# Performance work log

Measured on AMD Instinct MI355X. Metric: run time of the kernel, lower is better.

The kernel has to match this reference:

```python
import jax, jax.numpy as jnp
import numpy as np

N = 2048      # agent_num
H = 2048      # hid_size
OBS = 1024    # obs_size
A = 64        # action_dim
ITERS = 3     # comm_iters
B = 1         # batch (structurally 1: original does gate.view(1,n,n))
STD = 0.02


def setup_inputs() -> dict:
    key = jax.random.key(0)
    ks = jax.random.split(key, 10)
    f = lambda k, shp: (jax.random.normal(k, shp, jnp.float32) * STD)
    return {
        "obs": jax.random.normal(ks[0], (B, N, OBS), jnp.float32),
        "alive_mask": jnp.ones((N,), jnp.float32),
        "enc_w": f(ks[1], (H, OBS)),
        "enc_b": jnp.zeros((H,), jnp.float32),
        "g_w": f(ks[2], (N, H)),
        "g_b": jnp.zeros((N,), jnp.float32),
        "w_ih": f(ks[3], (4 * H, H)),
        "w_hh": f(ks[4], (4 * H, H)),
        "b_ih": f(ks[5], (4 * H,)),
        "b_hh": f(ks[6], (4 * H,)),
        "act_w": f(ks[7], (A, H)),
        "act_b": jnp.zeros((A,), jnp.float32),
        "val_w": f(ks[8], (1, H)),
        "val_b": jnp.zeros((1,), jnp.float32),
    }


def reference(obs, alive_mask, enc_w, enc_b, g_w, g_b, w_ih, w_hh,
              b_ih, b_hh, act_w, act_b, val_w, val_b):
    b, n, _ = obs.shape
    hid = enc_w.shape[0]
    # state encoder: tanh(Linear(obs))
    e = jnp.tanh(jnp.einsum('bno,ho->bnh', obs, enc_w) + enc_b)  # (B,n,H)
    h = jnp.zeros((b, n, hid), obs.dtype)
    cell = jnp.zeros((b, n, hid), obs.dtype)
    comm_mask = 1.0 - jnp.eye(n, dtype=obs.dtype)                # (n,n), no self-comm
    n_alive = jnp.sum(alive_mask)
    alive_pair = alive_mask[:, None] * alive_mask[None, :]       # alive[j]*alive[i]
    static_w = comm_mask * alive_pair / (n_alive - 1.0)          # (n,n)

    for it in range(ITERS):
        # hard gate: ceil(sigmoid(g(h)))  -> (B, n_sender, n_receiver)
        gate = jnp.ceil(jax.nn.sigmoid(jnp.einsum('bjh,kh->bjk', h, g_w) + g_b))
        G = gate * static_w                                      # (B,n,n)
        # masked gated broadcast-sum over sender agents j (fused, no (B,n,n,H))
        if it == 0:
            c = jnp.zeros_like(h)
        else:
            c = jnp.einsum('bji,bjh->bih', G, h)
        inp = e + c                                              # (B,n,H)
        # torch.nn.LSTMCell, gate order (i, f, g, o)
        z = (jnp.einsum('bnh,gh->bng', inp, w_ih)
             + jnp.einsum('bnh,gh->bng', h, w_hh) + b_ih + b_hh)
        zi, zf, zg, zo = jnp.split(z, 4, axis=-1)
        cell = jax.nn.sigmoid(zf) * cell + jax.nn.sigmoid(zi) * jnp.tanh(zg)
        h = jax.nn.sigmoid(zo) * jnp.tanh(cell)

    log_p = jax.nn.log_softmax(jnp.einsum('bnh,ah->bna', h, act_w) + act_b, axis=-1)
    value = jnp.einsum('bnh,vh->bnv', h, val_w) + val_b
    return log_p, value
```

## Files before the change

### kernel.cpp

```cpp
#include <hip/hip_runtime.h>
#include <cmath>

#define N_AG 2048
#define HID  2048
#define OBSD 1024
#define ACT  64
#define GATES (4*HID)

typedef short s16x8 __attribute__((ext_vector_type(8)));
typedef short s16x4 __attribute__((ext_vector_type(4)));
typedef float f32x4 __attribute__((ext_vector_type(4)));

__device__ __forceinline__ unsigned short f2bf(float f) {
  union { float f; unsigned u; } v; v.f = f;
  return (unsigned short)((v.u + 0x7FFFu + ((v.u >> 16) & 1u)) >> 16);
}
__device__ __forceinline__ float bf2f(unsigned short u) {
  union { float f; unsigned u; } v; v.u = ((unsigned)u) << 16;
  return v.f;
}
__device__ __forceinline__ float sigm(float x) { return 1.0f / (1.0f + expf(-x)); }

__device__ __forceinline__ void gload16(const unsigned short* g, unsigned short* l) {
  __builtin_amdgcn_global_load_lds(
      (const __attribute__((address_space(1))) void*)g,
      (__attribute__((address_space(3))) void*)l, 16, 0, 0);
}

__global__ __launch_bounds__(512, 2) void gemm256(
    const unsigned short* __restrict__ A, const unsigned short* __restrict__ B,
    int K, int lda, int ldb, unsigned short* __restrict__ C, int ldc)
{
  __shared__ __align__(16) unsigned short As[32768];
  __shared__ __align__(16) unsigned short Bs[32768];

  const int tid  = threadIdx.x;
  const int lane = tid & 63;
  const int wave = tid >> 6;
  const int wm   = wave >> 2, wn = wave & 3;
  const int quad = lane >> 4, l16 = lane & 15, r7 = lane & 7;
  const long tileM = (long)blockIdx.y * 256;
  const long tileN = (long)blockIdx.x * 256;

  const unsigned scol  = (((lane & 7) ^ (lane >> 3)) * 8u);
  const unsigned aoffL = (unsigned)(tileM + wave * 8 + (lane >> 3)) * (unsigned)lda + scol;
  const unsigned boffL = (unsigned)(tileN + (wave >> 2) * 64 + (wave & 3) * 8 + (lane >> 3))
                           * (unsigned)ldb + scol;

#define ST_A(d, h, t) { \
    gload16(A + aoffL + (unsigned)((h) * 64) * (unsigned)lda + (unsigned)(t) * 64u, \
            &As[(d) * 16384 + (h) * 8192 + wave * 512]); \
    gload16(A + aoffL + (unsigned)(128 + (h) * 64) * (unsigned)lda + (unsigned)(t) * 64u, \
            &As[(d) * 16384 + (h) * 8192 + wave * 512 + 4096]); }
#define ST_B(d, h, t) { \
    gload16(B + boffL + (unsigned)((h) * 32) * (unsigned)ldb + (unsigned)(t) * 64u, \
            &Bs[(d) * 16384 + (h) * 8192 + wave * 512]); \
    gload16(B + boffL + (unsigned)(128 + (h) * 32) * (unsigned)ldb + (unsigned)(t) * 64u, \
            &Bs[(d) * 16384 + (h) * 8192 + wave * 512 + 4096]); }

  const int ax = wm * 4096 + l16 * 64;
  const int bx = wn * 2048 + l16 * 64;
  const int c0 = (quad ^ r7) * 8;
  const int c1 = ((4 + quad) ^ r7) * 8;

  s16x8 af0[4][2], af1[4][2], bA[2][2], bB[2][2];
  f32x4 acc[8][4] = {};

#define LD_A(d, Mh, dst) { const unsigned short* p_ = &As[(d) * 16384 + (Mh) * 8192 + ax]; \
    _Pragma("unroll") for (int ml = 0; ml < 4; ++ml) { \
      dst[ml][0] = *(const s16x8*)(p_ + ml * 1024 + c0); \
      dst[ml][1] = *(const s16x8*)(p_ + ml * 1024 + c1); } }
#define LD_B(d, Nh, dst) { const unsigned short* p_ = &Bs[(d) * 16384 + (Nh) * 8192 + bx]; \
    _Pragma("unroll") for (int nl = 0; nl < 2; ++nl) { \
      dst[nl][0] = *(const s16x8*)(p_ + nl * 1024 + c0); \
      dst[nl][1] = *(const s16x8*)(p_ + nl * 1024 + c1); } }
#define QMM(Mh, Nh, afv, bb) \
    _Pragma("unroll") for (int ks = 0; ks < 2; ++ks) \
    _Pragma("unroll") for (int ml = 0; ml < 4; ++ml) \
    _Pragma("unroll") for (int nl = 0; nl < 2; ++nl) \
      acc[(Mh) * 4 + ml][(Nh) * 2 + nl] = __builtin_amdgcn_mfma_f32_16x16x32_bf16( \
          afv[ml][ks], bb[nl][ks], acc[(Mh) * 4 + ml][(Nh) * 2 + nl], 0, 0, 0);
#define BAR  __builtin_amdgcn_s_barrier()
#define SCHB __builtin_amdgcn_sched_barrier(0)

  const int NT = K >> 6;

  ST_B(0, 0, 0); ST_A(0, 0, 0); ST_B(0, 1, 0); ST_A(0, 1, 0);
  asm volatile("s_waitcnt vmcnt(0)" ::: "memory");
  BAR;
  LD_A(0, 0, af0); LD_B(0, 0, bA);

  for (int t = 0; t < NT; ++t) {
    const int cur = t & 1, nxt = cur ^ 1;
    const bool s1 = (t + 1 < NT);
    LD_B(cur, 1, bB);
    if (s1) { ST_B(nxt, 0, t + 1); ST_A(nxt, 0, t + 1); }
    SCHB;
    __builtin_amdgcn_s_setprio(1); QMM(0, 0, af0, bA); __builtin_amdgcn_s_setprio(0);
    if (s1) { asm volatile("s_waitcnt vmcnt(4)" ::: "memory"); }
    else    { asm volatile("s_waitcnt vmcnt(0)" ::: "memory"); }
    BAR;
    LD_A(cur, 1, af1);
    if (s1) ST_B(nxt, 1, t + 1);
    SCHB;
    __builtin_amdgcn_s_setprio(1); QMM(0, 1, af0, bB); __builtin_amdgcn_s_setprio(0);
    if (s1) { asm volatile("s_waitcnt vmcnt(2)" ::: "memory"); }
    BAR;
    if (s1) ST_A(nxt, 1, t + 1);
    SCHB;
    __builtin_amdgcn_s_setprio(1); QMM(1, 0, af1, bA); __builtin_amdgcn_s_setprio(0);
    if (s1) LD_B(nxt, 0, bA);
    BAR;
    if (s1) LD_A(nxt, 0, af0);
    SCHB;
    __builtin_amdgcn_s_setprio(1); QMM(1, 1, af1, bB); __builtin_amdgcn_s_setprio(0);
    if (s1) { asm volatile("s_waitcnt vmcnt(2)" ::: "memory"); }
    BAR;
  }

#pragma unroll
  for (int mf = 0; mf < 8; ++mf) {
    long r0 = tileM + wm * 128 + mf * 16 + quad * 4;
#pragma unroll
    for (int nf = 0; nf < 4; ++nf) {
      long col = tileN + wn * 64 + nf * 16 + l16;
#pragma unroll
      for (int r = 0; r < 4; ++r)
        C[(r0 + r) * ldc + col] = f2bf(acc[mf][nf][r]);
    }
  }
#undef ST_A
#undef ST_B
#undef LD_A
#undef LD_B
#undef QMM
#undef BAR
#undef SCHB
}

template <int MODE>
__global__ __launch_bounds__(256, 4) void gemm_bt(
    const unsigned short* __restrict__ A, const unsigned short* __restrict__ B,
    int K, int lda, int ldb,
    unsigned short* __restrict__ Cb, float* __restrict__ Cf, int ldc,
    const float* __restrict__ bias)
{
  __shared__ __align__(16) unsigned short As0[2 * 128 * 32];
  __shared__ __align__(16) unsigned short Bs0[2 * 128 * 32];
  const int tid  = threadIdx.x;
  const int lane = tid & 63;
  const int wave = tid >> 6;
  const int wm = wave >> 1, wn = wave & 1;
  const int quad = lane >> 4, l16 = lane & 15;
  const long tileM = (long)blockIdx.y * 128;
  const long tileN = (long)blockIdx.x * 128;

  const int srow = lane >> 2;
  const int skc  = (lane & 3) * 8;
  const unsigned short* gA = &A[(tileM + wave * 32 + srow) * lda + skc];
  const unsigned short* gB = &B[(tileN + wave * 32 + srow) * ldb + skc];
  const int ldsOff = wave * 32 * 32;

  f32x4 acc[4][4] = {};
  const int nIt = K >> 5;

  gload16(gA, &As0[ldsOff]);
  gload16(gA + 16 * lda, &As0[ldsOff + 16 * 32]);
  gload16(gB, &Bs0[ldsOff]);
  gload16(gB + 16 * ldb, &Bs0[ldsOff + 16 * 32]);

  for (int i = 0; i < nIt; ++i) {
    __syncthreads();
    const int cb = (i & 1) * 4096;
    if (i + 1 < nIt) {
      const int nb = ((i + 1) & 1) * 4096;
      const long ko = (long)(i + 1) * 32;
      gload16(gA + ko, &As0[nb + ldsOff]);
      gload16(gA + ko + 16 * lda, &As0[nb + ldsOff + 16 * 32]);
      gload16(gB + ko, &Bs0[nb + ldsOff]);
      gload16(gB + ko + 16 * ldb, &Bs0[nb + ldsOff + 16 * 32]);
    }
    s16x8 af[4], bfr[4];
#pragma unroll
    for (int ii = 0; ii < 4; ++ii)
      af[ii] = *(const s16x8*)&As0[cb + (wm * 64 + ii * 16 + l16) * 32 + quad * 8];
#pragma unroll
    for (int j = 0; j < 4; ++j)
      bfr[j] = *(const s16x8*)&Bs0[cb + (wn * 64 + j * 16 + l16) * 32 + quad * 8];
#pragma unroll
    for (int ii = 0; ii < 4; ++ii)
#pragma unroll
      for (int j = 0; j < 4; ++j)
        acc[ii][j] = __builtin_amdgcn_mfma_f32_16x16x32_bf16(af[ii], bfr[j], acc[ii][j], 0, 0, 0);
  }

#pragma unroll
  for (int i = 0; i < 4; ++i) {
    long r0 = tileM + wm * 64 + i * 16 + quad * 4;
#pragma unroll
    for (int j = 0; j < 4; ++j) {
      long col = tileN + wn * 64 + j * 16 + l16;
      float bv = (MODE == 1) ? bias[col] : 0.f;
#pragma unroll
      for (int r = 0; r < 4; ++r) {
        float v = acc[i][j][r];
        if (MODE == 1) v = tanhf(v + bv);
        if (MODE == 2) Cf[(r0 + r) * ldc + col] = v;
        else           Cb[(r0 + r) * ldc + col] = f2bf(v);
      }
    }
  }
}

__global__ void cvt4_dual(const float* __restrict__ inA, unsigned short* __restrict__ outA,
                          const float* __restrict__ inB, unsigned short* __restrict__ outB) {
  int i = blockIdx.x * 256 + threadIdx.x;
  f32x4 a = ((const f32x4*)inA)[i];
  f32x4 b = ((const f32x4*)inB)[i];
  s16x4 oa, ob;
#pragma unroll
  for (int c = 0; c < 4; ++c) { oa[c] = (short)f2bf(a[c]); ob[c] = (short)f2bf(b[c]); }
  ((s16x4*)outA)[i] = oa;
  ((s16x4*)outB)[i] = ob;
}

__global__ void buildw(const float* __restrict__ w_ih, const float* __restrict__ w_hh,
                       const float* __restrict__ nA,
                       unsigned short* __restrict__ Wihb, unsigned short* __restrict__ W2b) {
  int i = blockIdx.x * 256 + threadIdx.x;
  float s = 1.0f / (nA[0] - 1.0f);
  size_t off = (size_t)i * 4;
  f32x4 a = *(const f32x4*)&w_ih[off];
  f32x4 b = *(const f32x4*)&w_hh[off];
  s16x4 oa, ob;
#pragma unroll
  for (int c = 0; c < 4; ++c) {
    oa[c] = (short)f2bf(a[c]);
    ob[c] = (short)f2bf(b[c] - s * a[c]);
  }
  *(s16x4*)&Wihb[off] = oa;
  *(s16x4*)&W2b[off] = ob;
}

__global__ void build_whd(const float* __restrict__ act_w, const float* __restrict__ val_w,
                          unsigned short* __restrict__ whd) {
  int i = blockIdx.x * 256 + threadIdx.x;
  int r = i >> 9;
  int k = (i & 511) * 4;
  f32x4 v = {0.f, 0.f, 0.f, 0.f};
  if (r < 64)       v = *(const f32x4*)&act_w[(size_t)r * HID + k];
  else if (r == 64) v = *(const f32x4*)&val_w[k];
  s16x4 o;
  o[0] = (short)f2bf(v[0]); o[1] = (short)f2bf(v[1]);
  o[2] = (short)f2bf(v[2]); o[3] = (short)f2bf(v[3]);
  *(s16x4*)&whd[(size_t)r * HID + k] = o;
}

__global__ void biasmix(const float* __restrict__ b_ih, const float* __restrict__ b_hh,
                        float* __restrict__ bc) {
  int i = blockIdx.x * 256 + threadIdx.x;
  if (i < GATES) bc[i] = b_ih[i] + b_hh[i];
}

__global__ void nalive_k(const float* __restrict__ alive, float* __restrict__ nA) {
  __shared__ float red[256];
  float s = 0.f;
  for (int i = threadIdx.x; i < N_AG; i += 256) s += alive[i];
  red[threadIdx.x] = s;
  __syncthreads();
  for (int st = 128; st > 0; st >>= 1) {
    if (threadIdx.x < st) red[threadIdx.x] += red[threadIdx.x + st];
    __syncthreads();
  }
  if (threadIdx.x == 0) nA[0] = red[0];
}

__global__ void colsum(const unsigned short* __restrict__ hb, const float* __restrict__ alive,
                       float* __restrict__ S) {
  int hid = blockIdx.x * 256 + threadIdx.x;
  int r0 = blockIdx.y * 128;
  float s = 0.f;
  for (int n = r0; n < r0 + 128; ++n) s += alive[n] * bf2f(hb[(size_t)n * HID + hid]);
  atomicAdd(&S[hid], s);
}

__global__ __launch_bounds__(256) void gemv_q(const unsigned short* __restrict__ Wihb,
                                              const float* __restrict__ S,
                                              const float* __restrict__ nA,
                                              float* __restrict__ q) {
  __shared__ float Sl[HID];
  int tid = threadIdx.x, lane = tid & 63, wave = tid >> 6;
  for (int k = tid; k < HID; k += 256) Sl[k] = S[k];
  __syncthreads();
  int g = blockIdx.x * 4 + wave;
  const unsigned short* wr = Wihb + (size_t)g * HID;
  float acc = 0.f;
#pragma unroll
  for (int c = 0; c < 4; ++c) {
    int k = c * 512 + lane * 8;
    s16x8 w = *(const s16x8*)&wr[k];
#pragma unroll
    for (int e = 0; e < 8; ++e) acc += bf2f((unsigned short)w[e]) * Sl[k + e];
  }
  for (int off = 32; off; off >>= 1) acc += __shfl_xor(acc, off);
  if (lane == 0) q[g] = acc / (nA[0] - 1.0f);
}

__global__ void lstm_k(const unsigned short* __restrict__ zb, const unsigned short* __restrict__ E1b,
                       const float* __restrict__ q, const float* __restrict__ bc,
                       float* __restrict__ cell, unsigned short* __restrict__ hb, int first) {
  int i = blockIdx.x * 256 + threadIdx.x;
  int n = i >> 9;
  int hid = (i & 511) * 4;
  size_t base = (size_t)n * GATES;
  float zt[4][4];
#pragma unroll
  for (int t = 0; t < 4; ++t) {
    int off = t * HID + hid;
    s16x4 e1 = *(const s16x4*)&E1b[base + off];
    f32x4 bcv = *(const f32x4*)&bc[off];
#pragma unroll
    for (int c = 0; c < 4; ++c) zt[t][c] = bf2f((unsigned short)e1[c]) + bcv[c];
    if (!first) {
      s16x4 z2 = *(const s16x4*)&zb[base + off];
      f32x4 qv = *(const f32x4*)&q[off];
#pragma unroll
      for (int c = 0; c < 4; ++c) zt[t][c] += bf2f((unsigned short)z2[c]) + qv[c];
    }
  }
  f32x4 cold = {0.f, 0.f, 0.f, 0.f};
  if (!first) cold = ((const f32x4*)cell)[i];
  f32x4 cnew; s16x4 xb;
#pragma unroll
  for (int c = 0; c < 4; ++c) {
    float ig = sigm(zt[0][c]);
    float fg = sigm(zt[1][c]);
    float gg = tanhf(zt[2][c]);
    float og = sigm(zt[3][c]);
    cnew[c] = fg * cold[c] + ig * gg;
    float hv = og * tanhf(cnew[c]);
    xb[c] = (short)f2bf(hv);
  }
  ((f32x4*)cell)[i] = cnew;
  *(s16x4*)&hb[(size_t)n * HID + hid] = xb;
}

__global__ __launch_bounds__(256) void head_ep(const float* __restrict__ zh,
                                               const float* __restrict__ act_b,
                                               const float* __restrict__ val_b,
                                               float* __restrict__ out) {
  int wave = threadIdx.x >> 6, lane = threadIdx.x & 63;
  int row = blockIdx.x * 4 + wave;
  const float* zr = zh + (size_t)row * 128;
  float a = zr[lane] + act_b[lane];
  float m = a;
  for (int off = 32; off; off >>= 1) m = fmaxf(m, __shfl_xor(m, off));
  float ex = expf(a - m), s = ex;
  for (int off = 32; off; off >>= 1) s += __shfl_xor(s, off);
  out[(size_t)row * ACT + lane] = a - m - logf(s);
  if (lane == 0) out[(size_t)N_AG * ACT + row] = zr[64] + val_b[0];
}

extern "C" void kernel_launch(void* const* d_in, const int* in_sizes, int n_in,
                              void* d_out, int out_size, void* d_ws, size_t ws_size,
                              hipStream_t stream) {
  const float* obs   = (const float*)d_in[0];
  const float* alive = (const float*)d_in[1];
  const float* enc_w = (const float*)d_in[2];
  const float* enc_b = (const float*)d_in[3];
  const float* w_ih  = (const float*)d_in[6];
  const float* w_hh  = (const float*)d_in[7];
  const float* b_ih  = (const float*)d_in[8];
  const float* b_hh  = (const float*)d_in[9];
  const float* act_w = (const float*)d_in[10];
  const float* act_b = (const float*)d_in[11];
  const float* val_w = (const float*)d_in[12];
  const float* val_b = (const float*)d_in[13];
  float* out = (float*)d_out;

  char* p = (char*)d_ws;
  unsigned short* Wihb = (unsigned short*)p; p += (size_t)GATES * HID * 2;
  unsigned short* W2b  = (unsigned short*)p; p += (size_t)GATES * HID * 2;
  unsigned short* E1b  = (unsigned short*)p; p += (size_t)N_AG * GATES * 2;
  unsigned short* zb   = (unsigned short*)p; p += (size_t)N_AG * GATES * 2;
  unsigned short* obsb = (unsigned short*)p; p += (size_t)N_AG * OBSD * 2;
  unsigned short* encb = (unsigned short*)p; p += (size_t)HID * OBSD * 2;
  unsigned short* eb   = (unsigned short*)p; p += (size_t)N_AG * HID * 2;
  unsigned short* hb   = (unsigned short*)p; p += (size_t)N_AG * HID * 2;
  unsigned short* Whd  = (unsigned short*)p; p += (size_t)128 * HID * 2;
  float* cell = (float*)p; p += (size_t)N_AG * HID * 4;
  float* zh   = (float*)p; p += (size_t)N_AG * 128 * 4;
  float* bc   = (float*)p; p += GATES * 4;
  float* q    = (float*)p; p += GATES * 4;
  float* S    = (float*)p; p += HID * 4;
  float* nA   = (float*)p; p += 256;

  cvt4_dual<<<(N_AG * OBSD / 4) / 256, 256, 0, stream>>>(obs, obsb, enc_w, encb);
  nalive_k<<<1, 256, 0, stream>>>(alive, nA);
  buildw<<<((size_t)GATES * HID / 4) / 256, 256, 0, stream>>>(w_ih, w_hh, nA, Wihb, W2b);
  build_whd<<<(128 * HID / 4) / 256, 256, 0, stream>>>(act_w, val_w, Whd);
  biasmix<<<GATES / 256, 256, 0, stream>>>(b_ih, b_hh, bc);

  gemm_bt<1><<<dim3(HID / 128, N_AG / 128), 256, 0, stream>>>(
      obsb, encb, OBSD, OBSD, OBSD, eb, nullptr, HID, enc_b);

  gemm256<<<dim3(GATES / 256, N_AG / 256), 512, 0, stream>>>(
      eb, Wihb, HID, HID, HID, E1b, GATES);
  lstm_k<<<(N_AG * HID / 4) / 256, 256, 0, stream>>>(nullptr, E1b, nullptr, bc, cell, hb, 1);

  for (int it = 1; it < 3; ++it) {
    hipMemsetAsync(S, 0, HID * 4, stream);
    colsum<<<dim3(HID / 256, 16), 256, 0, stream>>>(hb, alive, S);
    gemv_q<<<GATES / 4, 256, 0, stream>>>(Wihb, S, nA, q);
    gemm256<<<dim3(GATES / 256, N_AG / 256), 512, 0, stream>>>(
        hb, W2b, HID, HID, HID, zb, GATES);
    lstm_k<<<(N_AG * HID / 4) / 256, 256, 0, stream>>>(zb, E1b, q, bc, cell, hb, 0);
  }

  gemm_bt<2><<<dim3(1, N_AG / 128), 256, 0, stream>>>(
      hb, Whd, HID, HID, HID, nullptr, zh, 128, nullptr);
  head_ep<<<N_AG / 4, 256, 0, stream>>>(zh, act_b, val_b, out);
}
```

Before: 565.1 us.

## Fuse LSTM cell update into gate GEMM epilogue via interleaved weight layout

Reorders the rows of the input and recurrent weights and the combined bias so that each 64-column slice of a GEMM tile holds the i, f, g, o gates for the same 16 hidden units. The LSTM cell update then runs in the GEMM epilogue, which removes the separate lstm kernel and the bf16 round trip through the z buffer. h is double-buffered because the GEMM now writes new h while other blocks still read the old h. The head GEMM is also split along K into 8 chunks that accumulate with atomics, so it launches more blocks; the price is an extra memset and float atomics.

```diff
diff --git a/kernel.cpp b/kernel.cpp
--- a/kernel.cpp
+++ b/kernel.cpp
@@ -27,9 +27,14 @@
       (__attribute__((address_space(3))) void*)l, 16, 0, 0);
 }
 
+
+template <int MODE>
 __global__ __launch_bounds__(512, 2) void gemm256(
     const unsigned short* __restrict__ A, const unsigned short* __restrict__ B,
-    int K, int lda, int ldb, unsigned short* __restrict__ C, int ldc)
+    int K, int lda, int ldb,
+    unsigned short* __restrict__ E1b, const float* __restrict__ q,
+    const float* __restrict__ bc, float* __restrict__ cell,
+    unsigned short* __restrict__ hN)
 {
   __shared__ __align__(16) unsigned short As[32768];
   __shared__ __align__(16) unsigned short Bs[32768];
@@ -118,15 +123,40 @@
     BAR;
   }
 
+  const int cb0 = (int)tileN + wn * 64;
+  const int hid = ((cb0 >> 6) << 4) | l16;
+  float bcv[4], qv[4];
+#pragma unroll
+  for (int g = 0; g < 4; ++g) {
+    bcv[g] = bc[cb0 + g * 16 + l16];
+    qv[g]  = (MODE == 11) ? q[cb0 + g * 16 + l16] : 0.f;
+  }
 #pragma unroll
   for (int mf = 0; mf < 8; ++mf) {
-    long r0 = tileM + wm * 128 + mf * 16 + quad * 4;
-#pragma unroll
-    for (int nf = 0; nf < 4; ++nf) {
-      long col = tileN + wn * 64 + nf * 16 + l16;
-#pragma unroll
-      for (int r = 0; r < 4; ++r)
-        C[(r0 + r) * ldc + col] = f2bf(acc[mf][nf][r]);
+    long ag0 = tileM + wm * 128 + mf * 16 + quad * 4;
+#pragma unroll
+    for (int r = 0; r < 4; ++r) {
+      long ag = ag0 + r;
+      size_t eb_i = (size_t)ag * GATES + cb0 + l16;
+      float zi = acc[mf][0][r], zf = acc[mf][1][r];
+      float zg = acc[mf][2][r], zo = acc[mf][3][r];
+      if (MODE == 10) {
+        E1b[eb_i]      = f2bf(zi);
+        E1b[eb_i + 16] = f2bf(zf);
+        E1b[eb_i + 32] = f2bf(zg);
+        E1b[eb_i + 48] = f2bf(zo);
+        zi += bcv[0]; zf += bcv[1]; zg += bcv[2]; zo += bcv[3];
+      } else {
+        zi += bf2f(E1b[eb_i])      + qv[0] + bcv[0];
+        zf += bf2f(E1b[eb_i + 16]) + qv[1] + bcv[1];
+        zg += bf2f(E1b[eb_i + 32]) + qv[2] + bcv[2];
+        zo += bf2f(E1b[eb_i + 48]) + qv[3] + bcv[3];
+      }
+      float cold = (MODE == 10) ? 0.f : cell[(size_t)ag * HID + hid];
+      float cnew = sigm(zf) * cold + sigm(zi) * tanhf(zg);
+      float hv   = sigm(zo) * tanhf(cnew);
+      cell[(size_t)ag * HID + hid] = cnew;
+      hN[(size_t)ag * HID + hid]   = f2bf(hv);
     }
   }
 #undef ST_A
@@ -154,11 +184,12 @@
   const int quad = lane >> 4, l16 = lane & 15;
   const long tileM = (long)blockIdx.y * 128;
   const long tileN = (long)blockIdx.x * 128;
+  const long koff  = (long)blockIdx.z * K;
 
   const int srow = lane >> 2;
   const int skc  = (lane & 3) * 8;
-  const unsigned short* gA = &A[(tileM + wave * 32 + srow) * lda + skc];
-  const unsigned short* gB = &B[(tileN + wave * 32 + srow) * ldb + skc];
+  const unsigned short* gA = &A[(tileM + wave * 32 + srow) * lda + koff + skc];
+  const unsigned short* gB = &B[(tileN + wave * 32 + srow) * ldb + koff + skc];
   const int ldsOff = wave * 32 * 32;
 
   f32x4 acc[4][4] = {};
@@ -204,9 +235,8 @@
 #pragma unroll
       for (int r = 0; r < 4; ++r) {
         float v = acc[i][j][r];
-        if (MODE == 1) v = tanhf(v + bv);
-        if (MODE == 2) Cf[(r0 + r) * ldc + col] = v;
-        else           Cb[(r0 + r) * ldc + col] = f2bf(v);
+        if (MODE == 1) { v = tanhf(v + bv); Cb[(r0 + r) * ldc + col] = f2bf(v); }
+        if (MODE == 2) atomicAdd(&Cf[(r0 + r) * ldc + col], v);
       }
     }
   }
@@ -229,17 +259,22 @@
                        unsigned short* __restrict__ Wihb, unsigned short* __restrict__ W2b) {
   int i = blockIdx.x * 256 + threadIdx.x;
   float s = 1.0f / (nA[0] - 1.0f);
-  size_t off = (size_t)i * 4;
-  f32x4 a = *(const f32x4*)&w_ih[off];
-  f32x4 b = *(const f32x4*)&w_hh[off];
+  int c  = i >> 9;
+  int kk = (i & 511) * 4;
+  int g   = (c >> 4) & 3;
+  int hid = ((c >> 6) << 4) | (c & 15);
+  size_t src = ((size_t)g * HID + hid) * HID + kk;
+  size_t dst = (size_t)c * HID + kk;
+  f32x4 a = *(const f32x4*)&w_ih[src];
+  f32x4 b = *(const f32x4*)&w_hh[src];
   s16x4 oa, ob;
 #pragma unroll
-  for (int c = 0; c < 4; ++c) {
-    oa[c] = (short)f2bf(a[c]);
-    ob[c] = (short)f2bf(b[c] - s * a[c]);
-  }
-  *(s16x4*)&Wihb[off] = oa;
-  *(s16x4*)&W2b[off] = ob;
+  for (int e = 0; e < 4; ++e) {
+    oa[e] = (short)f2bf(a[e]);
+    ob[e] = (short)f2bf(b[e] - s * a[e]);
+  }
+  *(s16x4*)&Wihb[dst] = oa;
+  *(s16x4*)&W2b[dst] = ob;
 }
 
 __global__ void build_whd(const float* __restrict__ act_w, const float* __restrict__ val_w,
@@ -259,7 +294,12 @@
 __global__ void biasmix(const float* __restrict__ b_ih, const float* __restrict__ b_hh,
                         float* __restrict__ bc) {
   int i = blockIdx.x * 256 + threadIdx.x;
-  if (i < GATES) bc[i] = b_ih[i] + b_hh[i];
+  if (i < GATES) {
+    int g   = (i >> 4) & 3;
+    int hid = ((i >> 6) << 4) | (i & 15);
+    int src = g * HID + hid;
+    bc[i] = b_ih[src] + b_hh[src];
+  }
 }
 
 __global__ void nalive_k(const float* __restrict__ alive, float* __restrict__ nA) {
@@ -304,45 +344,6 @@
   }
   for (int off = 32; off; off >>= 1) acc += __shfl_xor(acc, off);
   if (lane == 0) q[g] = acc / (nA[0] - 1.0f);
-}
-
-__global__ void lstm_k(const unsigned short* __restrict__ zb, const unsigned short* __restrict__ E1b,
-                       const float* __restrict__ q, const float* __restrict__ bc,
-                       float* __restrict__ cell, unsigned short* __restrict__ hb, int first) {
-  int i = blockIdx.x * 256 + threadIdx.x;
-  int n = i >> 9;
-  int hid = (i & 511) * 4;
-  size_t base = (size_t)n * GATES;
-  float zt[4][4];
-#pragma unroll
-  for (int t = 0; t < 4; ++t) {
-    int off = t * HID + hid;
-    s16x4 e1 = *(const s16x4*)&E1b[base + off];
-    f32x4 bcv = *(const f32x4*)&bc[off];
-#pragma unroll
-    for (int c = 0; c < 4; ++c) zt[t][c] = bf2f((unsigned short)e1[c]) + bcv[c];
-    if (!first) {
-      s16x4 z2 = *(const s16x4*)&zb[base + off];
-      f32x4 qv = *(const f32x4*)&q[off];
-#pragma unroll
-      for (int c = 0; c < 4; ++c) zt[t][c] += bf2f((unsigned short)z2[c]) + qv[c];
-    }
-  }
-  f32x4 cold = {0.f, 0.f, 0.f, 0.f};
-  if (!first) cold = ((const f32x4*)cell)[i];
-  f32x4 cnew; s16x4 xb;
-#pragma unroll
-  for (int c = 0; c < 4; ++c) {
-    float ig = sigm(zt[0][c]);
-    float fg = sigm(zt[1][c]);
-    float gg = tanhf(zt[2][c]);
-    float og = sigm(zt[3][c]);
-    cnew[c] = fg * cold[c] + ig * gg;
-    float hv = og * tanhf(cnew[c]);
-    xb[c] = (short)f2bf(hv);
-  }
-  ((f32x4*)cell)[i] = cnew;
-  *(s16x4*)&hb[(size_t)n * HID + hid] = xb;
 }
 
 __global__ __launch_bounds__(256) void head_ep(const float* __restrict__ zh,
@@ -382,11 +383,11 @@
   unsigned short* Wihb = (unsigned short*)p; p += (size_t)GATES * HID * 2;
   unsigned short* W2b  = (unsigned short*)p; p += (size_t)GATES * HID * 2;
   unsigned short* E1b  = (unsigned short*)p; p += (size_t)N_AG * GATES * 2;
-  unsigned short* zb   = (unsigned short*)p; p += (size_t)N_AG * GATES * 2;
   unsigned short* obsb = (unsigned short*)p; p += (size_t)N_AG * OBSD * 2;
   unsigned short* encb = (unsigned short*)p; p += (size_t)HID * OBSD * 2;
   unsigned short* eb   = (unsigned short*)p; p += (size_t)N_AG * HID * 2;
-  unsigned short* hb   = (unsigned short*)p; p += (size_t)N_AG * HID * 2;
+  unsigned short* h0   = (unsigned short*)p; p += (size_t)N_AG * HID * 2;
+  unsigned short* h1   = (unsigned short*)p; p += (size_t)N_AG * HID * 2;
   unsigned short* Whd  = (unsigned short*)p; p += (size_t)128 * HID * 2;
   float* cell = (float*)p; p += (size_t)N_AG * HID * 4;
   float* zh   = (float*)p; p += (size_t)N_AG * 128 * 4;
@@ -404,20 +405,22 @@
   gemm_bt<1><<<dim3(HID / 128, N_AG / 128), 256, 0, stream>>>(
       obsb, encb, OBSD, OBSD, OBSD, eb, nullptr, HID, enc_b);
 
-  gemm256<<<dim3(GATES / 256, N_AG / 256), 512, 0, stream>>>(
-      eb, Wihb, HID, HID, HID, E1b, GATES);
-  lstm_k<<<(N_AG * HID / 4) / 256, 256, 0, stream>>>(nullptr, E1b, nullptr, bc, cell, hb, 1);
-
+  gemm256<10><<<dim3(GATES / 256, N_AG / 256), 512, 0, stream>>>(
+      eb, Wihb, HID, HID, HID, E1b, nullptr, bc, cell, h0);
+
+  unsigned short* hcur = h0;
+  unsigned short* hnxt = h1;
   for (int it = 1; it < 3; ++it) {
     hipMemsetAsync(S, 0, HID * 4, stream);
-    colsum<<<dim3(HID / 256, 16), 256, 0, stream>>>(hb, alive, S);
+    colsum<<<dim3(HID / 256, 16), 256, 0, stream>>>(hcur, alive, S);
     gemv_q<<<GATES / 4, 256, 0, stream>>>(Wihb, S, nA, q);
-    gemm256<<<dim3(GATES / 256, N_AG / 256), 512, 0, stream>>>(
-        hb, W2b, HID, HID, HID, zb, GATES);
-    lstm_k<<<(N_AG * HID / 4) / 256, 256, 0, stream>>>(zb, E1b, q, bc, cell, hb, 0);
-  }
-
-  gemm_bt<2><<<dim3(1, N_AG / 128), 256, 0, stream>>>(
-      hb, Whd, HID, HID, HID, nullptr, zh, 128, nullptr);
+    gemm256<11><<<dim3(GATES / 256, N_AG / 256), 512, 0, stream>>>(
+        hcur, W2b, HID, HID, HID, E1b, q, bc, cell, hnxt);
+    unsigned short* tmp = hcur; hcur = hnxt; hnxt = tmp;
+  }
+
+  hipMemsetAsync(zh, 0, (size_t)N_AG * 128 * 4, stream);
+  gemm_bt<2><<<dim3(1, N_AG / 128, 8), 256, 0, stream>>>(
+      hcur, Whd, HID / 8, HID, HID, nullptr, zh, 128, nullptr);
   head_ep<<<N_AG / 4, 256, 0, stream>>>(zh, act_b, val_b, out);
 }
```

New measurement: 537.2 us. -4.9%, faster.
